# Kernel optimization log

Measured on AMD Instinct MI355X. Metric: run time of the kernel, lower is better.

The kernel has to match this reference:

```python
import jax, jax.numpy as jnp
import numpy as np

HIDDEN = 1024
N_EXPERTS = 8
CAP_FACTOR = 1.1
LN_EPS = 1e-5


def setup_inputs() -> dict:
    key = jax.random.key(0)
    ks = jax.random.split(key, 8)
    d, E, dff = HIDDEN, N_EXPERTS, 4 * HIDDEN
    x = jax.random.normal(ks[0], (4, 2048, d), dtype=jnp.float32)
    gate_w = jax.random.normal(ks[1], (d, E), dtype=jnp.float32) / np.sqrt(d)
    ln_g = jnp.ones((E, d), dtype=jnp.float32)
    ln_b = jnp.zeros((E, d), dtype=jnp.float32)
    w1 = jax.random.normal(ks[2], (E, d, dff), dtype=jnp.float32) / np.sqrt(d)
    b1 = jnp.zeros((E, dff), dtype=jnp.float32)
    w2 = jax.random.normal(ks[3], (E, dff, d), dtype=jnp.float32) / np.sqrt(dff)
    b2 = jnp.zeros((E, d), dtype=jnp.float32)
    return {"x": x, "gate_w": gate_w, "ln_g": ln_g, "ln_b": ln_b,
            "w1": w1, "b1": b1, "w2": w2, "b2": b2}


def reference(x, gate_w, ln_g, ln_b, w1, b1, w2, b2):
    B, S, d = x.shape
    E = gate_w.shape[1]
    N = B * S
    cap = int(N / E * CAP_FACTOR)  # expert capacity

    xt = x.reshape(N, d)
    # Router: top-1 expert per token (max-subtract before softmax is a no-op)
    logits = xt @ gate_w                               # [N, E]
    probs = jax.nn.softmax(logits, axis=-1)
    eidx = jnp.argmax(probs, axis=-1)                  # [N] int

    onehot = jax.nn.one_hot(eidx, E, dtype=jnp.int32)  # [N, E]
    counts = onehot.sum(axis=0).astype(jnp.float32)    # pre-drop counts [E]

    # Deterministic capacity: keep first `cap` tokens per expert, drop rest.
    # (torch code drops randomly via multinomial; structure is identical.)
    pos = jnp.cumsum(onehot, axis=0) - 1               # [N, E]
    pos_tok = jnp.take_along_axis(pos, eidx[:, None], axis=1)[:, 0]  # [N]
    keep = (pos_tok < cap).astype(x.dtype)             # [N]
    pos_c = jnp.minimum(pos_tok, cap - 1)              # clamp; dropped tokens write zeros

    # Dispatch into per-expert buffers [E, cap, d]
    buf = jnp.zeros((E, cap, d), dtype=x.dtype).at[eidx, pos_c].add(xt * keep[:, None])

    # Per-expert FFN: LayerNorm -> Linear -> GELU -> Linear
    mu = buf.mean(axis=-1, keepdims=True)
    var = jnp.mean((buf - mu) ** 2, axis=-1, keepdims=True)
    nb = (buf - mu) * jax.lax.rsqrt(var + LN_EPS)
    nb = nb * ln_g[:, None, :] + ln_b[:, None, :]
    h = jax.nn.gelu(jnp.einsum('ecd,edf->ecf', nb, w1) + b1[:, None, :], approximate=False)
    y = jnp.einsum('ecf,efd->ecd', h, w2) + b2[:, None, :]  # [E, cap, d]

    # Combine: dropped tokens get zeros (matches torch output init)
    out_tok = y[eidx, pos_c] * keep[:, None]           # [N, d]
    output = out_tok.reshape(B, S, d)

    # Load-balancing loss: 1 - cosine(counts, uniform) * 0.01
    tokens_per_expert = N / E
    uniform = jnp.full((E,), tokens_per_expert, dtype=jnp.float32)
    cos = jnp.dot(counts, uniform) / (jnp.linalg.norm(counts) * jnp.linalg.norm(uniform) + 1e-8)
    loss = 1.0 - cos * 0.01
    return output, loss
```

## Files before the change

kernel.cpp:

```cpp
#include <hip/hip_runtime.h>
#include <cstdint>
#include <cstddef>

#define NTOK 8192
#define D    1024
#define DFF  4096
#define NEXP 8
#define CAP  1126
#define MPAD 1152

typedef float f32x4 __attribute__((ext_vector_type(4)));
typedef __bf16 bf16x8 __attribute__((ext_vector_type(8)));

__device__ inline unsigned short f2bf(float f) {
    unsigned u = __float_as_uint(f);
    u += 0x7fffu + ((u >> 16) & 1u);
    return (unsigned short)(u >> 16);
}

__device__ inline float gelu(float x) {
    float z  = 0.70710678118654752f * x;
    float az = fabsf(z);
    float t  = 1.0f / fmaf(0.3275911f, az, 1.0f);
    float p  = t * fmaf(t, fmaf(t, fmaf(t, fmaf(t, 1.061405429f, -1.453152027f),
                                        1.421413741f), -0.284496736f), 0.254829592f);
    float ee = __expf(-az * az);
    float er = fmaf(-p, ee, 1.0f);
    er = __builtin_copysignf(er, z);
    return 0.5f * x * (1.0f + er);
}

__device__ inline void gload16(const void* g, void* l) {
    __builtin_amdgcn_global_load_lds(
        (const __attribute__((address_space(1))) unsigned int*)g,
        (__attribute__((address_space(3))) unsigned int*)l,
        16, 0, 0);
}

__device__ void transpose_tile_dev(const float* __restrict__ W, unsigned short* __restrict__ WT,
                                   int K, int N, int tb, char* smem)
{
    int tiles_k = K >> 7, tiles_n = N >> 7;
    int per_e = tiles_k * tiles_n;
    int e = tb / per_e, rem = tb % per_e;
    int kb = rem % tiles_k, nb = rem / tiles_k;
    const float* We = W + (size_t)e * K * N + (size_t)(kb * 128) * N + nb * 128;
    unsigned short* Oe = WT + (size_t)e * K * N + (size_t)(nb * 128) * K + kb * 128;
    float* lds = (float*)smem;
    int t = threadIdx.x;
    #pragma unroll
    for (int p = 0; p < 2; ++p) {
        __syncthreads();
        #pragma unroll
        for (int j = 0; j < 8; ++j) {
            int idx = j * 256 + t;
            int r = idx >> 5, c4 = idx & 31;
            const float4 v = *(const float4*)(We + (size_t)(p * 64 + r) * N + c4 * 4);
            *(float4*)(lds + r * 128 + c4 * 4) = v;
        }
        __syncthreads();
        int c = t >> 1, half = t & 1;
        const float* col = lds + (half * 32) * 128 + c;
        unsigned short* orow = Oe + (size_t)c * K + p * 64 + half * 32;
        #pragma unroll
        for (int q = 0; q < 4; ++q) {
            uint4 o;
            o.x = f2bf(col[(q*8+0)*128]) | ((unsigned)f2bf(col[(q*8+1)*128]) << 16);
            o.y = f2bf(col[(q*8+2)*128]) | ((unsigned)f2bf(col[(q*8+3)*128]) << 16);
            o.z = f2bf(col[(q*8+4)*128]) | ((unsigned)f2bf(col[(q*8+5)*128]) << 16);
            o.w = f2bf(col[(q*8+6)*128]) | ((unsigned)f2bf(col[(q*8+7)*128]) << 16);
            *(uint4*)(orow + q * 8) = o;
        }
    }
}

__global__ __launch_bounds__(256) void transpose_kernel(
    const float* __restrict__ W, unsigned short* __restrict__ WT, int K, int N)
{
    __shared__ __align__(16) char smem[32768];
    transpose_tile_dev(W, WT, K, N, blockIdx.x, smem);
}

__global__ __launch_bounds__(256) void router_kernel(
    const float* __restrict__ x, const float* __restrict__ gw, int* __restrict__ eidx)
{
    int tok  = blockIdx.x * 4 + (threadIdx.x >> 6);
    int lane = threadIdx.x & 63;
    const float* xr = x + (size_t)tok * D;
    float a[8] = {0.f,0.f,0.f,0.f,0.f,0.f,0.f,0.f};
    #pragma unroll
    for (int it = 0; it < D / 64; ++it) {
        int d = lane + it * 64;
        float xv = xr[d];
        const float4 g0 = *(const float4*)(gw + (size_t)d * 8);
        const float4 g1 = *(const float4*)(gw + (size_t)d * 8 + 4);
        a[0] += xv * g0.x; a[1] += xv * g0.y; a[2] += xv * g0.z; a[3] += xv * g0.w;
        a[4] += xv * g1.x; a[5] += xv * g1.y; a[6] += xv * g1.z; a[7] += xv * g1.w;
    }
    #pragma unroll
    for (int off = 32; off > 0; off >>= 1)
        #pragma unroll
        for (int e = 0; e < 8; ++e) a[e] += __shfl_xor(a[e], off, 64);
    if (lane == 0) {
        int bi = 0; float bv = a[0];
        #pragma unroll
        for (int e = 1; e < 8; ++e) if (a[e] > bv) { bv = a[e]; bi = e; }
        eidx[tok] = bi;
    }
}

__global__ __launch_bounds__(1024) void scan_kernel(
    const int* __restrict__ eidx, int* __restrict__ slot_map,
    int* __restrict__ kept_cnt, float* __restrict__ loss_out,
    int* __restrict__ droplist, int* __restrict__ dropcnt)
{
    __shared__ int sc[8][1024];
    __shared__ int dcnt;
    int t = threadIdx.x;
    if (t == 0) dcnt = 0;
    int le[8];
    int c[8] = {0,0,0,0,0,0,0,0};
    #pragma unroll
    for (int i = 0; i < 8; ++i) { le[i] = eidx[t * 8 + i]; c[le[i]]++; }
    int v[8];
    #pragma unroll
    for (int e = 0; e < 8; ++e) { v[e] = c[e]; sc[e][t] = v[e]; }
    __syncthreads();
    for (int s = 1; s < 1024; s <<= 1) {
        int add[8] = {0,0,0,0,0,0,0,0};
        if (t >= s) {
            #pragma unroll
            for (int e = 0; e < 8; ++e) add[e] = sc[e][t - s];
        }
        __syncthreads();
        #pragma unroll
        for (int e = 0; e < 8; ++e) { v[e] += add[e]; sc[e][t] = v[e]; }
        __syncthreads();
    }
    int base[8];
    #pragma unroll
    for (int e = 0; e < 8; ++e) base[e] = v[e] - c[e];
    #pragma unroll
    for (int i = 0; i < 8; ++i) {
        int e = le[i]; int pos = base[e]++;
        if (pos < CAP) slot_map[e * CAP + pos] = t * 8 + i;
        else { int s = atomicAdd(&dcnt, 1); droplist[s] = t * 8 + i; }
    }
    __syncthreads();
    if (t == 0) *dropcnt = dcnt;
    if (t == 1023) {
        float dotv = 0.f, ss = 0.f;
        #pragma unroll
        for (int e = 0; e < 8; ++e) {
            float cf = (float)v[e];
            kept_cnt[e] = v[e] < CAP ? v[e] : CAP;
            dotv += cf * 1024.0f;
            ss   += cf * cf;
        }
        float denom = sqrtf(ss) * (1024.0f * sqrtf(8.0f)) + 1e-8f;
        loss_out[0] = 1.0f - 0.01f * (dotv / denom);
    }
}

__global__ __launch_bounds__(256) void zero_dropped(
    const int* __restrict__ droplist, const int* __restrict__ dropcnt,
    float4* __restrict__ out)
{
    int n = (*dropcnt) * 256;
    for (int idx = blockIdx.x * 256 + threadIdx.x; idx < n; idx += gridDim.x * 256)
        out[(size_t)droplist[idx >> 8] * 256 + (idx & 255)] = make_float4(0.f,0.f,0.f,0.f);
}

__global__ __launch_bounds__(256) void dispatch_ln(
    const float* __restrict__ x, const float* __restrict__ lng, const float* __restrict__ lnb,
    const int* __restrict__ slot_map, const int* __restrict__ kept_cnt,
    unsigned short* __restrict__ xbuf)
{
    int p = blockIdx.x, e = blockIdx.y, tid = threadIdx.x;
    ushort4* dst = (ushort4*)(xbuf + ((size_t)e * MPAD + p) * D) + tid;
    if (p >= kept_cnt[e]) { *dst = make_ushort4(0, 0, 0, 0); return; }
    int tok = slot_map[e * CAP + p];
    const float4 xv = *((const float4*)(x + (size_t)tok * D) + tid);
    float s  = xv.x + xv.y + xv.z + xv.w;
    float ss = xv.x * xv.x + xv.y * xv.y + xv.z * xv.z + xv.w * xv.w;
    #pragma unroll
    for (int off = 32; off > 0; off >>= 1) {
        s  += __shfl_xor(s,  off, 64);
        ss += __shfl_xor(ss, off, 64);
    }
    __shared__ float red[8];
    int lane = tid & 63, wv = tid >> 6;
    if (lane == 0) { red[wv] = s; red[4 + wv] = ss; }
    __syncthreads();
    s  = red[0] + red[1] + red[2] + red[3];
    ss = red[4] + red[5] + red[6] + red[7];
    float mu = s * (1.0f / D);
    float rs = rsqrtf(ss * (1.0f / D) - mu * mu + 1e-5f);
    const float4 gv = *((const float4*)(lng + (size_t)e * D) + tid);
    const float4 bv = *((const float4*)(lnb + (size_t)e * D) + tid);
    ushort4 o;
    o.x = f2bf((xv.x - mu) * rs * gv.x + bv.x);
    o.y = f2bf((xv.y - mu) * rs * gv.y + bv.y);
    o.z = f2bf((xv.z - mu) * rs * gv.z + bv.z);
    o.w = f2bf((xv.w - mu) * rs * gv.w + bv.w);
    *dst = o;
}

template<int K, int N, int MODE>
__global__ __launch_bounds__(256, 2) void gemm_kernel(
    const unsigned short* __restrict__ A,
    const unsigned short* __restrict__ BT,
    const float* __restrict__ bias,
    unsigned short* __restrict__ Hout,
    float* __restrict__ Yout,
    const int* __restrict__ slot_map,
    const int* __restrict__ kept_cnt)
{
    constexpr int MB = MPAD / 128;
    constexpr int NB = N / 128;
    constexpr int GB = NEXP * MB * NB;
    __shared__ __align__(16) char smem[65536];

    const int obid = blockIdx.x;
    const int q8 = GB >> 3, r8 = GB & 7;
    const int xcd = obid & 7, ii = obid >> 3;
    const int swz = (xcd < r8 ? xcd * (q8 + 1) : r8 * (q8 + 1) + (xcd - r8) * q8) + ii;
    const int mb = swz % MB;
    const int t2 = swz / MB;
    const int nb = t2 % NB;
    const int e  = t2 / NB;

    const int tid  = threadIdx.x;
    const int lane = tid & 63;
    const int l15  = lane & 15, lg = lane >> 4;
    const int wave = tid >> 6, wr = wave >> 1, wc = wave & 1;
    const unsigned short* Ae = A + ((size_t)e * MPAD + (size_t)mb * 128) * K;
    const unsigned short* Be = BT + ((size_t)e * N + (size_t)nb * 128) * K;
    f32x4 acc[4][4] = {};

    auto stage = [&](int buf, int kk) {
        char* sA = smem + buf * 32768;
        char* sB = sA + 16384;
        #pragma unroll
        for (int q = 0; q < 4; ++q) {
            int cid = q * 256 + tid;
            int row = cid >> 3, pp = cid & 7;
            int cc  = pp ^ ((row >> 1) & 7);
            gload16(Ae + (size_t)row * K + kk * 64 + cc * 8, sA + cid * 16);
            gload16(Be + (size_t)row * K + kk * 64 + cc * 8, sB + cid * 16);
        }
    };
    auto compute = [&](int buf) {
        const char* sA = smem + buf * 32768;
        const char* sB = sA + 16384;
        bf16x8 af[2][4], bfr[2][4];
        #pragma unroll
        for (int ks = 0; ks < 2; ++ks) {
            #pragma unroll
            for (int i = 0; i < 4; ++i) {
                int ra = wr * 64 + i * 16 + l15;
                af[ks][i]  = *(const bf16x8*)(sA + ra * 128 +
                             (((ks * 4 + lg) ^ ((ra >> 1) & 7)) << 4));
                int rb = wc * 64 + i * 16 + l15;
                bfr[ks][i] = *(const bf16x8*)(sB + rb * 128 +
                             (((ks * 4 + lg) ^ ((rb >> 1) & 7)) << 4));
            }
        }
        #pragma unroll
        for (int ks = 0; ks < 2; ++ks)
            #pragma unroll
            for (int mi = 0; mi < 4; ++mi)
                #pragma unroll
                for (int ni = 0; ni < 4; ++ni)
                    acc[mi][ni] = __builtin_amdgcn_mfma_f32_16x16x32_bf16(
                        bfr[ks][ni], af[ks][mi], acc[mi][ni], 0, 0, 0);
    };

    constexpr int T = K / 64;
    stage(0, 0);
    asm volatile("s_waitcnt vmcnt(0)" ::: "memory");
    __syncthreads();
    int cur = 0;
    for (int kk = 0; kk + 1 < T; ++kk) {
        stage(cur ^ 1, kk + 1);
        compute(cur);
        asm volatile("s_waitcnt vmcnt(0)" ::: "memory");
        __syncthreads();
        cur ^= 1;
    }
    compute(cur);

    const int kept = (MODE == 1) ? kept_cnt[e] : 0;
    #pragma unroll
    for (int mi = 0; mi < 4; ++mi) {
        const int row = mb * 128 + wr * 64 + mi * 16 + l15;
        int tok = 0; bool live = true;
        if (MODE == 1) {
            live = row < kept;
            tok = live ? slot_map[e * CAP + row] : 0;
        }
        #pragma unroll
        for (int ni = 0; ni < 4; ++ni) {
            const int colb = nb * 128 + wc * 64 + ni * 16 + 4 * lg;
            const float4 bv = *(const float4*)(bias + (size_t)e * N + colb);
            if (MODE == 0) {
                ushort4 o;
                o.x = f2bf(gelu(acc[mi][ni][0] + bv.x));
                o.y = f2bf(gelu(acc[mi][ni][1] + bv.y));
                o.z = f2bf(gelu(acc[mi][ni][2] + bv.z));
                o.w = f2bf(gelu(acc[mi][ni][3] + bv.w));
                *(ushort4*)(Hout + ((size_t)e * MPAD + row) * N + colb) = o;
            } else if (live) {
                float4 o = make_float4(acc[mi][ni][0] + bv.x, acc[mi][ni][1] + bv.y,
                                       acc[mi][ni][2] + bv.z, acc[mi][ni][3] + bv.w);
                *(float4*)(Yout + (size_t)tok * D + colb) = o;
            }
        }
    }
}

extern "C" void kernel_launch(void* const* d_in, const int* in_sizes, int n_in,
                              void* d_out, int out_size, void* d_ws, size_t ws_size,
                              hipStream_t stream)
{
    const float* x   = (const float*)d_in[0];
    const float* gw  = (const float*)d_in[1];
    const float* lng = (const float*)d_in[2];
    const float* lnb = (const float*)d_in[3];
    const float* w1  = (const float*)d_in[4];
    const float* b1  = (const float*)d_in[5];
    const float* w2  = (const float*)d_in[6];
    const float* b2  = (const float*)d_in[7];
    float* out = (float*)d_out;
    char* ws = (char*)d_ws;

    unsigned short* wT   = (unsigned short*)ws;
    unsigned short* xbuf = (unsigned short*)(ws + 67108864);
    unsigned short* hbuf = (unsigned short*)(ws + 67108864 + 18874368);
    int* eidx     = (int*)(ws + 161480704);
    int* slot_map = eidx + NTOK;
    int* kept     = slot_map + NEXP * CAP;
    int* dropcnt  = kept + NEXP;
    int* droplist = dropcnt + 8;

    constexpr int GB1 = NEXP * (MPAD / 128) * (DFF / 128);
    constexpr int GB2 = NEXP * (MPAD / 128) * (D / 128);
    constexpr int TB1 = NEXP * (D / 128) * (DFF / 128);
    constexpr int TB2 = NEXP * (DFF / 128) * (D / 128);

    router_kernel<<<NTOK / 4, 256, 0, stream>>>(x, gw, eidx);
    scan_kernel<<<1, 1024, 0, stream>>>(eidx, slot_map, kept,
                                        out + (size_t)NTOK * D, droplist, dropcnt);
    zero_dropped<<<64, 256, 0, stream>>>(droplist, dropcnt, (float4*)out);
    dispatch_ln<<<dim3(MPAD, NEXP), 256, 0, stream>>>(x, lng, lnb, slot_map, kept, xbuf);

    transpose_kernel<<<TB1, 256, 0, stream>>>(w1, wT, D, DFF);
    gemm_kernel<D, DFF, 0><<<GB1, 256, 0, stream>>>(
        xbuf, wT, b1, hbuf, nullptr, slot_map, kept);

    transpose_kernel<<<TB2, 256, 0, stream>>>(w2, wT, DFF, D);
    gemm_kernel<DFF, D, 1><<<GB2, 256, 0, stream>>>(
        hbuf, wT, b2, nullptr, out, slot_map, kept);
}
```

Baseline: 344.9 us.

## Use 256x256 GEMM tiles with 8 waves and two-deep LDS prefetch

Both expert GEMMs move from 128x128 tiles with 4 waves to 256x256 tiles with 8 waves and 128KB of LDS. The k-loop keeps two stages in flight, splits each step into four sub-tile load/MFMA phases, and raises wave priority around the MFMAs. The goal is more operand reuse per global load and more overlap of loads with matrix math. The cost is row padding rising from 1152 to 1280 per expert, far fewer blocks (160 for the second GEMM), and lower occupancy.

```diff
diff --git a/kernel.cpp b/kernel.cpp
--- a/kernel.cpp
+++ b/kernel.cpp
@@ -7,7 +7,7 @@
 #define DFF  4096
 #define NEXP 8
 #define CAP  1126
-#define MPAD 1152
+#define MROWS 1280
 
 typedef float f32x4 __attribute__((ext_vector_type(4)));
 typedef __bf16 bf16x8 __attribute__((ext_vector_type(8)));
@@ -177,7 +177,7 @@
     unsigned short* __restrict__ xbuf)
 {
     int p = blockIdx.x, e = blockIdx.y, tid = threadIdx.x;
-    ushort4* dst = (ushort4*)(xbuf + ((size_t)e * MPAD + p) * D) + tid;
+    ushort4* dst = (ushort4*)(xbuf + ((size_t)e * MROWS + p) * D) + tid;
     if (p >= kept_cnt[e]) { *dst = make_ushort4(0, 0, 0, 0); return; }
     int tok = slot_map[e * CAP + p];
     const float4 xv = *((const float4*)(x + (size_t)tok * D) + tid);
@@ -207,7 +207,7 @@
 }
 
 template<int K, int N, int MODE>
-__global__ __launch_bounds__(256, 2) void gemm_kernel(
+__global__ __launch_bounds__(512, 2) void gemm_kernel(
     const unsigned short* __restrict__ A,
     const unsigned short* __restrict__ BT,
     const float* __restrict__ bias,
@@ -216,10 +216,11 @@
     const int* __restrict__ slot_map,
     const int* __restrict__ kept_cnt)
 {
-    constexpr int MB = MPAD / 128;
-    constexpr int NB = N / 128;
+    constexpr int MB = MROWS / 256;
+    constexpr int NB = N / 256;
     constexpr int GB = NEXP * MB * NB;
-    __shared__ __align__(16) char smem[65536];
+    constexpr int T  = K / 64;
+    __shared__ __align__(16) char smem[131072];
 
     const int obid = blockIdx.x;
     const int q8 = GB >> 3, r8 = GB & 7;
@@ -233,67 +234,89 @@
     const int tid  = threadIdx.x;
     const int lane = tid & 63;
     const int l15  = lane & 15, lg = lane >> 4;
-    const int wave = tid >> 6, wr = wave >> 1, wc = wave & 1;
-    const unsigned short* Ae = A + ((size_t)e * MPAD + (size_t)mb * 128) * K;
-    const unsigned short* Be = BT + ((size_t)e * N + (size_t)nb * 128) * K;
-    f32x4 acc[4][4] = {};
-
-    auto stage = [&](int buf, int kk) {
-        char* sA = smem + buf * 32768;
-        char* sB = sA + 16384;
+    const int wave = tid >> 6;
+    const int wr = wave >> 2, wc = wave & 3;
+    const unsigned short* Ae = A + ((size_t)e * MROWS + (size_t)mb * 256) * K;
+    const unsigned short* Be = BT + ((size_t)e * N + (size_t)nb * 256) * K;
+    f32x4 acc[8][4] = {};
+
+    auto stageAB = [&](int buf, int kk) {
+        char* sA = smem + buf * 65536;
+        char* sB = sA + 32768;
         #pragma unroll
         for (int q = 0; q < 4; ++q) {
-            int cid = q * 256 + tid;
+            int cid = q * 512 + tid;
             int row = cid >> 3, pp = cid & 7;
             int cc  = pp ^ ((row >> 1) & 7);
             gload16(Ae + (size_t)row * K + kk * 64 + cc * 8, sA + cid * 16);
             gload16(Be + (size_t)row * K + kk * 64 + cc * 8, sB + cid * 16);
         }
     };
-    auto compute = [&](int buf) {
-        const char* sA = smem + buf * 32768;
-        const char* sB = sA + 16384;
-        bf16x8 af[2][4], bfr[2][4];
-        #pragma unroll
-        for (int ks = 0; ks < 2; ++ks) {
+    auto quad_load = [&](const char* sA, const char* sB, int mh, int nh,
+                         bf16x8 (&af)[2][4], bf16x8 (&bfv)[2][2]) {
+        #pragma unroll
+        for (int i = 0; i < 4; ++i) {
+            int ra = wr * 128 + mh * 64 + i * 16 + l15;
             #pragma unroll
-            for (int i = 0; i < 4; ++i) {
-                int ra = wr * 64 + i * 16 + l15;
-                af[ks][i]  = *(const bf16x8*)(sA + ra * 128 +
+            for (int ks = 0; ks < 2; ++ks)
+                af[ks][i] = *(const bf16x8*)(sA + ra * 128 +
                              (((ks * 4 + lg) ^ ((ra >> 1) & 7)) << 4));
-                int rb = wc * 64 + i * 16 + l15;
-                bfr[ks][i] = *(const bf16x8*)(sB + rb * 128 +
+        }
+        #pragma unroll
+        for (int jn = 0; jn < 2; ++jn) {
+            int rb = wc * 64 + nh * 32 + jn * 16 + l15;
+            #pragma unroll
+            for (int ks = 0; ks < 2; ++ks)
+                bfv[ks][jn] = *(const bf16x8*)(sB + rb * 128 +
                              (((ks * 4 + lg) ^ ((rb >> 1) & 7)) << 4));
-            }
-        }
+        }
+    };
+    auto quad_mfma = [&](int mh, int nh, bf16x8 (&af)[2][4], bf16x8 (&bfv)[2][2]) {
+        __builtin_amdgcn_s_setprio(1);
         #pragma unroll
         for (int ks = 0; ks < 2; ++ks)
             #pragma unroll
-            for (int mi = 0; mi < 4; ++mi)
+            for (int i = 0; i < 4; ++i)
                 #pragma unroll
-                for (int ni = 0; ni < 4; ++ni)
-                    acc[mi][ni] = __builtin_amdgcn_mfma_f32_16x16x32_bf16(
-                        bfr[ks][ni], af[ks][mi], acc[mi][ni], 0, 0, 0);
+                for (int jn = 0; jn < 2; ++jn)
+                    acc[mh * 4 + i][nh * 2 + jn] = __builtin_amdgcn_mfma_f32_16x16x32_bf16(
+                        bfv[ks][jn], af[ks][i], acc[mh * 4 + i][nh * 2 + jn], 0, 0, 0);
+        __builtin_amdgcn_s_setprio(0);
     };
 
-    constexpr int T = K / 64;
-    stage(0, 0);
-    asm volatile("s_waitcnt vmcnt(0)" ::: "memory");
-    __syncthreads();
-    int cur = 0;
-    for (int kk = 0; kk + 1 < T; ++kk) {
-        stage(cur ^ 1, kk + 1);
-        compute(cur);
-        asm volatile("s_waitcnt vmcnt(0)" ::: "memory");
-        __syncthreads();
-        cur ^= 1;
-    }
-    compute(cur);
+    stageAB(0, 0);
+    stageAB(1, 1);
+    asm volatile("s_waitcnt vmcnt(8)" ::: "memory");
+    __builtin_amdgcn_s_barrier();
+
+    for (int t = 0; t < T; ++t) {
+        const char* sA = smem + (t & 1) * 65536;
+        const char* sB = sA + 32768;
+        bf16x8 af[2][4]; bf16x8 bfv[2][2];
+        quad_load(sA, sB, 0, 0, af, bfv);  quad_mfma(0, 0, af, bfv);
+        __builtin_amdgcn_sched_barrier(0);
+        quad_load(sA, sB, 0, 1, af, bfv);  quad_mfma(0, 1, af, bfv);
+        __builtin_amdgcn_sched_barrier(0);
+        quad_load(sA, sB, 1, 0, af, bfv);  quad_mfma(1, 0, af, bfv);
+        __builtin_amdgcn_sched_barrier(0);
+        quad_load(sA, sB, 1, 1, af, bfv);
+        asm volatile("s_waitcnt lgkmcnt(0)" ::: "memory");
+        __builtin_amdgcn_sched_barrier(0);
+        __builtin_amdgcn_s_barrier();
+        if (t + 2 < T) stageAB(t & 1, t + 2);
+        __builtin_amdgcn_sched_barrier(0);
+        quad_mfma(1, 1, af, bfv);
+        if (t < T - 1) {
+            if (t + 2 < T) asm volatile("s_waitcnt vmcnt(8)" ::: "memory");
+            else           asm volatile("s_waitcnt vmcnt(0)" ::: "memory");
+            __builtin_amdgcn_s_barrier();
+        }
+    }
 
     const int kept = (MODE == 1) ? kept_cnt[e] : 0;
     #pragma unroll
-    for (int mi = 0; mi < 4; ++mi) {
-        const int row = mb * 128 + wr * 64 + mi * 16 + l15;
+    for (int mi = 0; mi < 8; ++mi) {
+        const int row = mb * 256 + wr * 128 + mi * 16 + l15;
         int tok = 0; bool live = true;
         if (MODE == 1) {
             live = row < kept;
@@ -301,7 +324,7 @@
         }
         #pragma unroll
         for (int ni = 0; ni < 4; ++ni) {
-            const int colb = nb * 128 + wc * 64 + ni * 16 + 4 * lg;
+            const int colb = nb * 256 + wc * 64 + ni * 16 + 4 * lg;
             const float4 bv = *(const float4*)(bias + (size_t)e * N + colb);
             if (MODE == 0) {
                 ushort4 o;
@@ -309,7 +332,7 @@
                 o.y = f2bf(gelu(acc[mi][ni][1] + bv.y));
                 o.z = f2bf(gelu(acc[mi][ni][2] + bv.z));
                 o.w = f2bf(gelu(acc[mi][ni][3] + bv.w));
-                *(ushort4*)(Hout + ((size_t)e * MPAD + row) * N + colb) = o;
+                *(ushort4*)(Hout + ((size_t)e * MROWS + row) * N + colb) = o;
             } else if (live) {
                 float4 o = make_float4(acc[mi][ni][0] + bv.x, acc[mi][ni][1] + bv.y,
                                        acc[mi][ni][2] + bv.z, acc[mi][ni][3] + bv.w);
@@ -336,15 +359,15 @@
 
     unsigned short* wT   = (unsigned short*)ws;
     unsigned short* xbuf = (unsigned short*)(ws + 67108864);
-    unsigned short* hbuf = (unsigned short*)(ws + 67108864 + 18874368);
-    int* eidx     = (int*)(ws + 161480704);
+    unsigned short* hbuf = (unsigned short*)(ws + 88080384);
+    int* eidx     = (int*)(ws + 171966464);
     int* slot_map = eidx + NTOK;
     int* kept     = slot_map + NEXP * CAP;
     int* dropcnt  = kept + NEXP;
     int* droplist = dropcnt + 8;
 
-    constexpr int GB1 = NEXP * (MPAD / 128) * (DFF / 128);
-    constexpr int GB2 = NEXP * (MPAD / 128) * (D / 128);
+    constexpr int GB1 = NEXP * (MROWS / 256) * (DFF / 256);
+    constexpr int GB2 = NEXP * (MROWS / 256) * (D / 256);
     constexpr int TB1 = NEXP * (D / 128) * (DFF / 128);
     constexpr int TB2 = NEXP * (DFF / 128) * (D / 128);
 
@@ -352,13 +375,13 @@
     scan_kernel<<<1, 1024, 0, stream>>>(eidx, slot_map, kept,
                                         out + (size_t)NTOK * D, droplist, dropcnt);
     zero_dropped<<<64, 256, 0, stream>>>(droplist, dropcnt, (float4*)out);
-    dispatch_ln<<<dim3(MPAD, NEXP), 256, 0, stream>>>(x, lng, lnb, slot_map, kept, xbuf);
+    dispatch_ln<<<dim3(MROWS, NEXP), 256, 0, stream>>>(x, lng, lnb, slot_map, kept, xbuf);
 
     transpose_kernel<<<TB1, 256, 0, stream>>>(w1, wT, D, DFF);
-    gemm_kernel<D, DFF, 0><<<GB1, 256, 0, stream>>>(
+    gemm_kernel<D, DFF, 0><<<GB1, 512, 0, stream>>>(
         xbuf, wT, b1, hbuf, nullptr, slot_map, kept);
 
     transpose_kernel<<<TB2, 256, 0, stream>>>(w2, wT, DFF, D);
-    gemm_kernel<DFF, D, 1><<<GB2, 256, 0, stream>>>(
+    gemm_kernel<DFF, D, 1><<<GB2, 512, 0, stream>>>(
         hbuf, wT, b2, nullptr, out, slot_map, kept);
 }
```

New measurement: 380.4 us. 10.3% more time.

## Use triple-buffered K=32 LDS pipeline in expert GEMM with higher occupancy

Applied to the files above, without the earlier changes.

The GEMM main loop now stages K=32 slices into three LDS buffers, keeping two tiles of loads in flight, where the old loop used K=64 slices in two buffers. It waits with partial vmcnt counts and raw s_barrier, and raises MFMA issue priority with s_setprio. With LDS cut from 64KB to 48KB, launch bounds go from 2 to 3 blocks per CU, which aims to hide global-load latency better. The risks are more barriers per K step, tighter register limits at higher occupancy, and correctness that depends on the exact vmcnt accounting. The transpose helper is folded into its kernel and the grid size is hardcoded to the same 2048 blocks.

```diff
diff --git a/kernel.cpp b/kernel.cpp
--- a/kernel.cpp
+++ b/kernel.cpp
@@ -37,9 +37,11 @@
         16, 0, 0);
 }
 
-__device__ void transpose_tile_dev(const float* __restrict__ W, unsigned short* __restrict__ WT,
-                                   int K, int N, int tb, char* smem)
-{
+__global__ __launch_bounds__(256) void transpose_kernel(
+    const float* __restrict__ W, unsigned short* __restrict__ WT, int K, int N)
+{
+    __shared__ __align__(16) char smem[32768];
+    int tb = blockIdx.x;
     int tiles_k = K >> 7, tiles_n = N >> 7;
     int per_e = tiles_k * tiles_n;
     int e = tb / per_e, rem = tb % per_e;
@@ -72,13 +74,6 @@
             *(uint4*)(orow + q * 8) = o;
         }
     }
-}
-
-__global__ __launch_bounds__(256) void transpose_kernel(
-    const float* __restrict__ W, unsigned short* __restrict__ WT, int K, int N)
-{
-    __shared__ __align__(16) char smem[32768];
-    transpose_tile_dev(W, WT, K, N, blockIdx.x, smem);
 }
 
 __global__ __launch_bounds__(256) void router_kernel(
@@ -207,7 +202,7 @@
 }
 
 template<int K, int N, int MODE>
-__global__ __launch_bounds__(256, 2) void gemm_kernel(
+__global__ __launch_bounds__(256, 3) void gemm_kernel(
     const unsigned short* __restrict__ A,
     const unsigned short* __restrict__ BT,
     const float* __restrict__ bias,
@@ -219,7 +214,8 @@
     constexpr int MB = MPAD / 128;
     constexpr int NB = N / 128;
     constexpr int GB = NEXP * MB * NB;
-    __shared__ __align__(16) char smem[65536];
+    constexpr int T  = K / 32;
+    __shared__ __align__(16) char smem[49152];
 
     const int obid = blockIdx.x;
     const int q8 = GB >> 3, r8 = GB & 7;
@@ -239,56 +235,59 @@
     f32x4 acc[4][4] = {};
 
     auto stage = [&](int buf, int kk) {
-        char* sA = smem + buf * 32768;
-        char* sB = sA + 16384;
-        #pragma unroll
-        for (int q = 0; q < 4; ++q) {
+        char* sA = smem + buf * 16384;
+        char* sB = sA + 8192;
+        #pragma unroll
+        for (int q = 0; q < 2; ++q) {
             int cid = q * 256 + tid;
-            int row = cid >> 3, pp = cid & 7;
-            int cc  = pp ^ ((row >> 1) & 7);
-            gload16(Ae + (size_t)row * K + kk * 64 + cc * 8, sA + cid * 16);
-            gload16(Be + (size_t)row * K + kk * 64 + cc * 8, sB + cid * 16);
+            int row = cid >> 2, pp = cid & 3;
+            int cc  = pp ^ ((row >> 1) & 3);
+            gload16(Ae + (size_t)row * K + kk * 32 + cc * 8, sA + cid * 16);
+            gload16(Be + (size_t)row * K + kk * 32 + cc * 8, sB + cid * 16);
         }
     };
     auto compute = [&](int buf) {
-        const char* sA = smem + buf * 32768;
-        const char* sB = sA + 16384;
-        bf16x8 af[2][4], bfr[2][4];
-        #pragma unroll
-        for (int ks = 0; ks < 2; ++ks) {
+        const char* sA = smem + buf * 16384;
+        const char* sB = sA + 8192;
+        bf16x8 af[4], bfr[4];
+        #pragma unroll
+        for (int i = 0; i < 4; ++i) {
+            int ra = wr * 64 + i * 16 + l15;
+            af[i]  = *(const bf16x8*)(sA + ra * 64 + ((lg ^ ((ra >> 1) & 3)) << 4));
+            int rb = wc * 64 + i * 16 + l15;
+            bfr[i] = *(const bf16x8*)(sB + rb * 64 + ((lg ^ ((rb >> 1) & 3)) << 4));
+        }
+        __builtin_amdgcn_s_setprio(1);
+        #pragma unroll
+        for (int mi = 0; mi < 4; ++mi)
             #pragma unroll
-            for (int i = 0; i < 4; ++i) {
-                int ra = wr * 64 + i * 16 + l15;
-                af[ks][i]  = *(const bf16x8*)(sA + ra * 128 +
-                             (((ks * 4 + lg) ^ ((ra >> 1) & 7)) << 4));
-                int rb = wc * 64 + i * 16 + l15;
-                bfr[ks][i] = *(const bf16x8*)(sB + rb * 128 +
-                             (((ks * 4 + lg) ^ ((rb >> 1) & 7)) << 4));
-            }
-        }
-        #pragma unroll
-        for (int ks = 0; ks < 2; ++ks)
-            #pragma unroll
-            for (int mi = 0; mi < 4; ++mi)
-                #pragma unroll
-                for (int ni = 0; ni < 4; ++ni)
-                    acc[mi][ni] = __builtin_amdgcn_mfma_f32_16x16x32_bf16(
-                        bfr[ks][ni], af[ks][mi], acc[mi][ni], 0, 0, 0);
+            for (int ni = 0; ni < 4; ++ni)
+                acc[mi][ni] = __builtin_amdgcn_mfma_f32_16x16x32_bf16(
+                    bfr[ni], af[mi], acc[mi][ni], 0, 0, 0);
+        __builtin_amdgcn_s_setprio(0);
     };
 
-    constexpr int T = K / 64;
     stage(0, 0);
-    asm volatile("s_waitcnt vmcnt(0)" ::: "memory");
-    __syncthreads();
-    int cur = 0;
-    for (int kk = 0; kk + 1 < T; ++kk) {
-        stage(cur ^ 1, kk + 1);
-        compute(cur);
-        asm volatile("s_waitcnt vmcnt(0)" ::: "memory");
-        __syncthreads();
-        cur ^= 1;
-    }
-    compute(cur);
+    stage(1, 1);
+    asm volatile("s_waitcnt vmcnt(4)" ::: "memory");
+    __builtin_amdgcn_s_barrier();
+    asm volatile("" ::: "memory");
+    int b = 0;
+    for (int t = 0; t < T - 2; ++t) {
+        int bn = b + 2; if (bn >= 3) bn -= 3;
+        stage(bn, t + 2);
+        compute(b);
+        asm volatile("s_waitcnt vmcnt(4) lgkmcnt(0)" ::: "memory");
+        __builtin_amdgcn_s_barrier();
+        asm volatile("" ::: "memory");
+        b = (b == 2) ? 0 : b + 1;
+    }
+    compute(b);
+    asm volatile("s_waitcnt vmcnt(0) lgkmcnt(0)" ::: "memory");
+    __builtin_amdgcn_s_barrier();
+    asm volatile("" ::: "memory");
+    b = (b == 2) ? 0 : b + 1;
+    compute(b);
 
     const int kept = (MODE == 1) ? kept_cnt[e] : 0;
     #pragma unroll
@@ -345,8 +344,7 @@
 
     constexpr int GB1 = NEXP * (MPAD / 128) * (DFF / 128);
     constexpr int GB2 = NEXP * (MPAD / 128) * (D / 128);
-    constexpr int TB1 = NEXP * (D / 128) * (DFF / 128);
-    constexpr int TB2 = NEXP * (DFF / 128) * (D / 128);
+    constexpr int TB  = 2048;
 
     router_kernel<<<NTOK / 4, 256, 0, stream>>>(x, gw, eidx);
     scan_kernel<<<1, 1024, 0, stream>>>(eidx, slot_map, kept,
@@ -354,11 +352,11 @@
     zero_dropped<<<64, 256, 0, stream>>>(droplist, dropcnt, (float4*)out);
     dispatch_ln<<<dim3(MPAD, NEXP), 256, 0, stream>>>(x, lng, lnb, slot_map, kept, xbuf);
 
-    transpose_kernel<<<TB1, 256, 0, stream>>>(w1, wT, D, DFF);
+    transpose_kernel<<<TB, 256, 0, stream>>>(w1, wT, D, DFF);
     gemm_kernel<D, DFF, 0><<<GB1, 256, 0, stream>>>(
         xbuf, wT, b1, hbuf, nullptr, slot_map, kept);
 
-    transpose_kernel<<<TB2, 256, 0, stream>>>(w2, wT, DFF, D);
+    transpose_kernel<<<TB, 256, 0, stream>>>(w2, wT, DFF, D);
     gemm_kernel<DFF, D, 1><<<GB2, 256, 0, stream>>>(
         hbuf, wT, b2, nullptr, out, slot_map, kept);
 }
```

After: 342.4 us. About the same (-0.7%).
